# Kernel optimization log

Measured on AMD Instinct MI355X. Metric: run time of the kernel, lower is better.

The kernel has to match this reference:

```python
import jax, jax.numpy as jnp
import numpy as np
from jax import lax

STATE_LEN = 5
N_BASE = 4
C = N_BASE ** STATE_LEN          # 1024 CRF states
NZ = N_BASE + 1                  # 5 incoming transitions per state
FEAT = 320
KW = 19
STRIDE = 5
SCALE = 5.0


def _transition_idx():
    # bonito CTC_CRF.idx: predecessor state for each (state, transition) pair
    a = np.arange(C)
    idx = np.concatenate([a[:, None], np.repeat(a, N_BASE).reshape(N_BASE, -1).T], axis=1)
    return jnp.asarray(idx, dtype=jnp.int32)  # [C, NZ]


def setup_inputs() -> dict:
    key = jax.random.key(0)
    ks = jax.random.split(key, 5)
    x = jax.random.normal(ks[0], (32, 1, 4000), jnp.float32)
    conv_w = jax.random.normal(ks[1], (FEAT, 1, KW), jnp.float32) * 0.1
    conv_b = jax.random.normal(ks[2], (FEAT,), jnp.float32) * 0.1
    lin_w = jax.random.normal(ks[3], (FEAT, C * NZ), jnp.float32) * (1.0 / np.sqrt(FEAT))
    lin_b = jax.random.normal(ks[4], (C * NZ,), jnp.float32) * 0.1
    return {"x": x, "conv_w": conv_w, "conv_b": conv_b, "lin_w": lin_w, "lin_b": lin_b}


def _encoder(x, conv_w, conv_b, lin_w, lin_b):
    # x: [N, 1, L] -> strided conv -> [N, FEAT, T]
    y = lax.conv_general_dilated(x, conv_w, (STRIDE,), "SAME",
                                 dimension_numbers=("NCH", "OIH", "NCH"))
    y = jnp.tanh(y + conv_b[None, :, None])
    y = jnp.transpose(y, (2, 0, 1))  # [T, N, FEAT]
    # scaled-tanh CRF output head -> [T, N, C*NZ]
    return SCALE * jnp.tanh(jnp.einsum("tnf,fc->tnc", y, lin_w) + lin_b)


def _logZ(scores, idx):
    # log-semiring forward algorithm (alpha_0 = beta_T = 0)
    T, N, _ = scores.shape
    Ms = scores.reshape(T, N, C, NZ)
    alpha0 = jnp.zeros((N, C), scores.dtype)

    def step(alpha, Ms_t):  # Ms_t: [N, C, NZ], alpha: [N, C]
        return jax.nn.logsumexp(Ms_t + alpha[:, idx], axis=2), None

    alpha, _ = lax.scan(step, alpha0, Ms)
    return jax.nn.logsumexp(alpha, axis=1)  # [N]


def reference(x, conv_w, conv_b, lin_w, lin_b):
    idx = _transition_idx()
    scores = _encoder(x, conv_w, conv_b, lin_w, lin_b).astype(jnp.float32)  # [T, N, 5120]
    T = scores.shape[0]
    # GlobalNorm: scores - logZ / T, broadcast over time and channel dims
    return scores - _logZ(scores, idx)[:, None] / T
```

## Files before the change

kernel.cpp:

```cpp
#include <hip/hip_runtime.h>
#include <hip/hip_bf16.h>


typedef __attribute__((ext_vector_type(8))) short bf16x8;
typedef __attribute__((ext_vector_type(4))) float f32x4;

#define T_STEPS 800
#define NBATCH 32
#define FEAT 320
#define CNZ 5120
#define MROWS (T_STEPS * NBATCH)

__device__ __forceinline__ float fast_tanh(float x) {
    float e = exp2f(x * 2.8853900817779268f);
    return 1.0f - 2.0f * __builtin_amdgcn_rcpf(e + 1.0f);
}

__global__ __launch_bounds__(320) void conv_kernel(
    const float* __restrict__ x, const float* __restrict__ w,
    const float* __restrict__ b, __hip_bfloat16* __restrict__ y) {
    int m = blockIdx.x;
    int t = m >> 5, n = m & 31;
    int f = threadIdx.x;
    __shared__ float xs[19];
    int base = t * 5 - 7;
    if (f < 19) {
        int pos = base + f;
        xs[f] = (pos >= 0 && pos < 4000) ? x[n * 4000 + pos] : 0.0f;
    }
    __syncthreads();
    float acc = b[f];
#pragma unroll
    for (int k = 0; k < 19; ++k) acc = fmaf(xs[k], w[f * 19 + k], acc);
    y[(size_t)m * FEAT + f] = __float2bfloat16(fast_tanh(acc));
}

__global__ __launch_bounds__(256) void transpose_w(
    const float* __restrict__ W, __hip_bfloat16* __restrict__ Wt) {
    __shared__ float tile[64][65];
    int nb = blockIdx.x * 64, kb = blockIdx.y * 64;
    int tx = threadIdx.x & 63, ty = threadIdx.x >> 6;
#pragma unroll
    for (int r = 0; r < 64; r += 4)
        tile[ty + r][tx] = W[(size_t)(kb + ty + r) * CNZ + nb + tx];
    __syncthreads();
#pragma unroll
    for (int r = 0; r < 64; r += 4) {
        int nn = ty + r;
        Wt[(size_t)(nb + nn) * FEAT + kb + tx] = __float2bfloat16(tile[tx][nn]);
    }
}

#define GBM 128
#define GBN 128
#define GBK 64
#define LDK 72

__global__ __launch_bounds__(256) void gemm_kernel(
    const __hip_bfloat16* __restrict__ A,
    const __hip_bfloat16* __restrict__ Bt,
    const float* __restrict__ bias,
    float* __restrict__ out) {
    __shared__ __align__(16) short As[GBM * LDK];
    __shared__ __align__(16) short Bs[GBN * LDK];
    const int K = FEAT;
    int bm0 = blockIdx.x * GBM;
    int bn0 = blockIdx.y * GBN;
    int tid = threadIdx.x;
    int wave = tid >> 6, lane = tid & 63;
    int wm = (wave >> 1) * 64, wn = (wave & 1) * 64;
    int col = lane & 15, quad = lane >> 4;

    f32x4 acc[4][4];
#pragma unroll
    for (int i = 0; i < 4; ++i)
#pragma unroll
        for (int j = 0; j < 4; ++j) acc[i][j] = (f32x4){0.f, 0.f, 0.f, 0.f};

    for (int k0 = 0; k0 < K; k0 += GBK) {
#pragma unroll
        for (int p = 0; p < 4; ++p) {
            int i = p * 256 + tid;
            int row = i >> 3, cg = i & 7;
            *(int4*)&As[row * LDK + cg * 8] =
                *(const int4*)&A[(size_t)(bm0 + row) * K + k0 + cg * 8];
            *(int4*)&Bs[row * LDK + cg * 8] =
                *(const int4*)&Bt[(size_t)(bn0 + row) * K + k0 + cg * 8];
        }
        __syncthreads();
#pragma unroll
        for (int kk = 0; kk < GBK; kk += 32) {
            bf16x8 af[4], bfr[4];
#pragma unroll
            for (int i = 0; i < 4; ++i)
                af[i] = *(bf16x8*)&As[(wm + i * 16 + col) * LDK + kk + quad * 8];
#pragma unroll
            for (int j = 0; j < 4; ++j)
                bfr[j] = *(bf16x8*)&Bs[(wn + j * 16 + col) * LDK + kk + quad * 8];
#pragma unroll
            for (int i = 0; i < 4; ++i)
#pragma unroll
                for (int j = 0; j < 4; ++j)
                    acc[i][j] = __builtin_amdgcn_mfma_f32_16x16x32_bf16(
                        af[i], bfr[j], acc[i][j], 0, 0, 0);
        }
        __syncthreads();
    }
#pragma unroll
    for (int j = 0; j < 4; ++j) {
        int n_g = bn0 + wn + j * 16 + col;
        float bj = bias[n_g];
#pragma unroll
        for (int i = 0; i < 4; ++i) {
            int m_base = bm0 + wm + i * 16 + quad * 4;
#pragma unroll
            for (int r = 0; r < 4; ++r) {
                out[(size_t)(m_base + r) * CNZ + n_g] =
                    5.0f * fast_tanh(acc[i][j][r] + bj);
            }
        }
    }
}

__global__ __launch_bounds__(1024) void forward_kernel(
    const float* __restrict__ scores, float* __restrict__ corr) {
    __shared__ float A0[1024];
    __shared__ float A1[1024];
    const int c = threadIdx.x;
    const int n = blockIdx.x;
    const int q = c >> 2;
    const float L2E = 1.4426950408889634f;
    const float LN2 = 0.6931471805599453f;
    A0[c] = 0.0f;
    __syncthreads();
    const size_t tstride = (size_t)NBATCH * CNZ;
    const float* p = scores + (size_t)n * CNZ + c * 5;
    float s0 = p[0], s1 = p[1], s2 = p[2], s3 = p[3], s4 = p[4];
    for (int t = 0; t < T_STEPS; ++t) {
        const float* pn = p + tstride;
        float u0 = 0.f, u1 = 0.f, u2 = 0.f, u3 = 0.f, u4 = 0.f;
        if (t < T_STEPS - 1) { u0 = pn[0]; u1 = pn[1]; u2 = pn[2]; u3 = pn[3]; u4 = pn[4]; }
        float* cur = (t & 1) ? A1 : A0;
        float* nxt = (t & 1) ? A0 : A1;
        float x0 = s0 + cur[c];
        float x1 = s1 + cur[q];
        float x2 = s2 + cur[q + 256];
        float x3 = s3 + cur[q + 512];
        float x4 = s4 + cur[q + 768];
        float mx = fmaxf(fmaxf(fmaxf(x0, x1), fmaxf(x2, x3)), x4);
        float sum = exp2f((x0 - mx) * L2E) + exp2f((x1 - mx) * L2E) +
                    exp2f((x2 - mx) * L2E) + exp2f((x3 - mx) * L2E) +
                    exp2f((x4 - mx) * L2E);
        nxt[c] = fmaf(log2f(sum), LN2, mx);
        __syncthreads();
        p = pn; s0 = u0; s1 = u1; s2 = u2; s3 = u3; s4 = u4;
    }
    float v = A0[c];
    A1[c] = v;
    __syncthreads();
    for (int s = 512; s > 0; s >>= 1) {
        if (c < s) A1[c] = fmaxf(A1[c], A1[c + s]);
        __syncthreads();
    }
    float mx = A1[0];
    __syncthreads();
    A1[c] = exp2f((v - mx) * L2E);
    __syncthreads();
    for (int s = 512; s > 0; s >>= 1) {
        if (c < s) A1[c] += A1[c + s];
        __syncthreads();
    }
    if (c == 0)
        corr[n] = fmaf(log2f(A1[0]), LN2, mx) * (1.0f / (float)T_STEPS);
}

__global__ __launch_bounds__(256) void sub_kernel(
    float* __restrict__ out, const float* __restrict__ corr) {
    size_t i4 = (size_t)blockIdx.x * blockDim.x + threadIdx.x;
    float cc = corr[(i4 / (CNZ / 4)) & (NBATCH - 1)];
    float4* o4 = (float4*)out;
    float4 v = o4[i4];
    v.x -= cc; v.y -= cc; v.z -= cc; v.w -= cc;
    o4[i4] = v;
}

extern "C" void kernel_launch(void* const* d_in, const int* in_sizes, int n_in,
                              void* d_out, int out_size, void* d_ws, size_t ws_size,
                              hipStream_t stream) {
    const float* x      = (const float*)d_in[0];
    const float* conv_w = (const float*)d_in[1];
    const float* conv_b = (const float*)d_in[2];
    const float* lin_w  = (const float*)d_in[3];
    const float* lin_b  = (const float*)d_in[4];
    float* out = (float*)d_out;

    char* ws = (char*)d_ws;
    __hip_bfloat16* y  = (__hip_bfloat16*)ws;
    __hip_bfloat16* wt = (__hip_bfloat16*)(ws + 16384000);
    float* corr        = (float*)(ws + 16384000 + 3276800);

    conv_kernel<<<MROWS, 320, 0, stream>>>(x, conv_w, conv_b, y);
    transpose_w<<<dim3(CNZ / 64, FEAT / 64), 256, 0, stream>>>(lin_w, wt);
    gemm_kernel<<<dim3(MROWS / GBM, CNZ / GBN), 256, 0, stream>>>(y, wt, lin_b, out);
    forward_kernel<<<NBATCH, 1024, 0, stream>>>(out, corr);
    sub_kernel<<<(out_size / 4) / 256, 256, 0, stream>>>(out, corr);
}
```

Measured before the change: 1.365 ms.

## Restructure CRF forward scan: 4 states per thread, deep prefetch, log2-domain

The forward recursion kernel now uses 256 threads per batch instead of 1024. Each thread handles 4 consecutive states, which share the same 4 predecessor alphas, so shared-memory reads are cut and stores become float4. Score loads are vectorised as float4 and prefetched 4 timesteps ahead in rotating register buffers, so global latency is hidden behind the serial scan. Alpha is kept in log2 units with hardware exp2/log intrinsics to shorten the math, at the cost of more registers and lower thread-level parallelism per block.

```diff
diff --git a/kernel.cpp b/kernel.cpp
--- a/kernel.cpp
+++ b/kernel.cpp
@@ -122,56 +122,92 @@
     }
 }
 
-__global__ __launch_bounds__(1024) void forward_kernel(
+
+__device__ __forceinline__ float lse5_2(float s0, float s1, float s2, float s3,
+                                        float s4, float a0, float a1, float a2,
+                                        float a3, float a4) {
+    const float L2E = 1.4426950408889634f;
+    float x0 = fmaf(s0, L2E, a0);
+    float x1 = fmaf(s1, L2E, a1);
+    float x2 = fmaf(s2, L2E, a2);
+    float x3 = fmaf(s3, L2E, a3);
+    float x4 = fmaf(s4, L2E, a4);
+    float mx = fmaxf(fmaxf(fmaxf(x0, x1), fmaxf(x2, x3)), x4);
+    float sum = __builtin_amdgcn_exp2f(x0 - mx) + __builtin_amdgcn_exp2f(x1 - mx) +
+                __builtin_amdgcn_exp2f(x2 - mx) + __builtin_amdgcn_exp2f(x3 - mx) +
+                __builtin_amdgcn_exp2f(x4 - mx);
+    return __builtin_amdgcn_logf(sum) + mx;
+}
+
+#define LOADP(P, TT) do {                                                      \
+    int tc_ = (TT) < T_STEPS ? (TT) : (T_STEPS - 1);                           \
+    const float4* p4_ = (const float4*)(base + (size_t)tc_ * tstride);         \
+    P[0] = p4_[0]; P[1] = p4_[1]; P[2] = p4_[2]; P[3] = p4_[3]; P[4] = p4_[4]; \
+} while (0)
+
+#define FSTEP(P, TT, cur, nxt) do {                                            \
+    float s0_ = P[0].x, s1_ = P[0].y, s2_ = P[0].z, s3_ = P[0].w, s4_ = P[1].x;\
+    float t0_ = P[1].y, t1_ = P[1].z, t2_ = P[1].w, t3_ = P[2].x, t4_ = P[2].y;\
+    float u0_ = P[2].z, u1_ = P[2].w, u2_ = P[3].x, u3_ = P[3].y, u4_ = P[3].z;\
+    float v0_ = P[3].w, v1_ = P[4].x, v2_ = P[4].y, v3_ = P[4].z, v4_ = P[4].w;\
+    LOADP(P, TT);                                                              \
+    float aq0_ = (cur)[tid], aq1_ = (cur)[tid + 256];                          \
+    float aq2_ = (cur)[tid + 512], aq3_ = (cur)[tid + 768];                    \
+    float4 ao_ = *(const float4*)&(cur)[4 * tid];                              \
+    float4 r_;                                                                 \
+    r_.x = lse5_2(s0_, s1_, s2_, s3_, s4_, ao_.x, aq0_, aq1_, aq2_, aq3_);     \
+    r_.y = lse5_2(t0_, t1_, t2_, t3_, t4_, ao_.y, aq0_, aq1_, aq2_, aq3_);     \
+    r_.z = lse5_2(u0_, u1_, u2_, u3_, u4_, ao_.z, aq0_, aq1_, aq2_, aq3_);     \
+    r_.w = lse5_2(v0_, v1_, v2_, v3_, v4_, ao_.w, aq0_, aq1_, aq2_, aq3_);     \
+    *(float4*)&(nxt)[4 * tid] = r_;                                            \
+    __syncthreads();                                                           \
+} while (0)
+
+__global__ __launch_bounds__(256) void forward_kernel(
     const float* __restrict__ scores, float* __restrict__ corr) {
     __shared__ float A0[1024];
     __shared__ float A1[1024];
-    const int c = threadIdx.x;
+    const int tid = threadIdx.x;
     const int n = blockIdx.x;
-    const int q = c >> 2;
-    const float L2E = 1.4426950408889634f;
     const float LN2 = 0.6931471805599453f;
-    A0[c] = 0.0f;
-    __syncthreads();
+
+    *(float4*)&A0[4 * tid] = (float4){0.f, 0.f, 0.f, 0.f};
+    __syncthreads();
+
     const size_t tstride = (size_t)NBATCH * CNZ;
-    const float* p = scores + (size_t)n * CNZ + c * 5;
-    float s0 = p[0], s1 = p[1], s2 = p[2], s3 = p[3], s4 = p[4];
-    for (int t = 0; t < T_STEPS; ++t) {
-        const float* pn = p + tstride;
-        float u0 = 0.f, u1 = 0.f, u2 = 0.f, u3 = 0.f, u4 = 0.f;
-        if (t < T_STEPS - 1) { u0 = pn[0]; u1 = pn[1]; u2 = pn[2]; u3 = pn[3]; u4 = pn[4]; }
-        float* cur = (t & 1) ? A1 : A0;
-        float* nxt = (t & 1) ? A0 : A1;
-        float x0 = s0 + cur[c];
-        float x1 = s1 + cur[q];
-        float x2 = s2 + cur[q + 256];
-        float x3 = s3 + cur[q + 512];
-        float x4 = s4 + cur[q + 768];
-        float mx = fmaxf(fmaxf(fmaxf(x0, x1), fmaxf(x2, x3)), x4);
-        float sum = exp2f((x0 - mx) * L2E) + exp2f((x1 - mx) * L2E) +
-                    exp2f((x2 - mx) * L2E) + exp2f((x3 - mx) * L2E) +
-                    exp2f((x4 - mx) * L2E);
-        nxt[c] = fmaf(log2f(sum), LN2, mx);
-        __syncthreads();
-        p = pn; s0 = u0; s1 = u1; s2 = u2; s3 = u3; s4 = u4;
-    }
-    float v = A0[c];
-    A1[c] = v;
-    __syncthreads();
-    for (int s = 512; s > 0; s >>= 1) {
-        if (c < s) A1[c] = fmaxf(A1[c], A1[c + s]);
+    const float* base = scores + (size_t)n * CNZ + tid * 20;
+
+    float4 P0[5], P1[5], P2[5], P3[5];
+    LOADP(P0, 0); LOADP(P1, 1); LOADP(P2, 2); LOADP(P3, 3);
+
+    for (int t = 0; t < T_STEPS; t += 4) {
+        FSTEP(P0, t + 4, A0, A1);
+        FSTEP(P1, t + 5, A1, A0);
+        FSTEP(P2, t + 6, A0, A1);
+        FSTEP(P3, t + 7, A1, A0);
+    }
+    float4 v = *(const float4*)&A0[4 * tid];
+    float pm = fmaxf(fmaxf(v.x, v.y), fmaxf(v.z, v.w));
+    A1[tid] = pm;
+    __syncthreads();
+#pragma unroll
+    for (int s = 128; s > 0; s >>= 1) {
+        if (tid < s) A1[tid] = fmaxf(A1[tid], A1[tid + s]);
         __syncthreads();
     }
     float mx = A1[0];
     __syncthreads();
-    A1[c] = exp2f((v - mx) * L2E);
-    __syncthreads();
-    for (int s = 512; s > 0; s >>= 1) {
-        if (c < s) A1[c] += A1[c + s];
-        __syncthreads();
-    }
-    if (c == 0)
-        corr[n] = fmaf(log2f(A1[0]), LN2, mx) * (1.0f / (float)T_STEPS);
+    float ps = __builtin_amdgcn_exp2f(v.x - mx) + __builtin_amdgcn_exp2f(v.y - mx) +
+               __builtin_amdgcn_exp2f(v.z - mx) + __builtin_amdgcn_exp2f(v.w - mx);
+    A1[tid] = ps;
+    __syncthreads();
+#pragma unroll
+    for (int s = 128; s > 0; s >>= 1) {
+        if (tid < s) A1[tid] += A1[tid + s];
+        __syncthreads();
+    }
+    if (tid == 0)
+        corr[n] = (__builtin_amdgcn_logf(A1[0]) + mx) * LN2 * (1.0f / (float)T_STEPS);
 }
 
 __global__ __launch_bounds__(256) void sub_kernel(
@@ -202,6 +238,6 @@
     conv_kernel<<<MROWS, 320, 0, stream>>>(x, conv_w, conv_b, y);
     transpose_w<<<dim3(CNZ / 64, FEAT / 64), 256, 0, stream>>>(lin_w, wt);
     gemm_kernel<<<dim3(MROWS / GBM, CNZ / GBN), 256, 0, stream>>>(y, wt, lin_b, out);
-    forward_kernel<<<NBATCH, 1024, 0, stream>>>(out, corr);
+    forward_kernel<<<NBATCH, 256, 0, stream>>>(out, corr);
     sub_kernel<<<(out_size / 4) / 256, 256, 0, stream>>>(out, corr);
 }
```

New measurement: 1.432 ms. 4.9% more time.
